# Performance work log

Hardware: AMD Instinct MI355X
Metric: run time of the kernel (lower is better)

## Reference

```python
import jax, jax.numpy as jnp
import numpy as np

B, N, C, S, H = 16, 4096, 512, 8, 8


def setup_inputs() -> dict:
    key = jax.random.key(0)
    ks = jax.random.split(key, 5)
    return {
        "x": jax.random.normal(ks[0], (B, N, C), jnp.float32),
        "w_sum": jax.random.normal(ks[1], (S, C), jnp.float32) * 0.02,
        "b_sum": jnp.zeros((S,), jnp.float32),
        "w_qkv": jax.random.normal(ks[2], (3 * C, C), jnp.float32) * 0.02,
        "w_cross": jax.random.normal(ks[3], (S, S), jnp.float32) * 0.02,
        "gamma": jnp.ones((C,), jnp.float32),
        "beta": jnp.zeros((C,), jnp.float32),
    }


def reference(x, w_sum, b_sum, w_qkv, w_cross, gamma, beta):
    Bx, Nx, Cx = x.shape
    hd = Cx // H
    scale = hd ** -0.5

    space_attn = x @ w_sum.T + b_sum                       # (B,N,S)
    # torch .view(B,C,N) on a (B,N,C) contiguous tensor is a memory
    # reinterpretation, NOT a transpose -> reshape then transpose.
    x_e = x.reshape(Bx, Cx, Nx).transpose(0, 2, 1)         # (B,N,C) reinterpreted
    sa = space_attn.reshape(Bx, S, Nx).transpose(0, 2, 1)  # (B,N,S) reinterpreted

    sa_soft = jax.nn.softmax(sa, axis=1)                   # softmax over N
    # broadcast multiply -> (B,N,S,C), top-1 over N == max over N
    tokens = jnp.max(sa_soft[:, :, :, None] * x_e[:, :, None, :], axis=1)  # (B,S,C)

    qkv = (tokens @ w_qkv.T).reshape(Bx, S, 3, H, hd).transpose(2, 0, 3, 1, 4)
    q, k, v = qkv[0], qkv[1], qkv[2]                       # (B,H,S,hd)
    attn = jax.nn.softmax(jnp.einsum('bhqd,bhkd->bhqk', q, k) * scale, axis=-1)
    asp = jnp.einsum('bhqk,bhkd->bhqd', attn, v)           # (B,H,S,hd)
    asp = asp.transpose(0, 2, 1, 3).reshape(Bx, S, Cx)     # (B,S,C)
    asp = (asp.transpose(0, 2, 1) @ w_cross.T).transpose(0, 2, 1)  # (B,S,C)

    # final mixing uses the PRE-softmax reinterpreted space_attn (as in torch)
    out = jnp.einsum('bns,bsc->bnc', sa, asp)              # (B,N,C)

    mu = out.mean(-1, keepdims=True)
    var = out.var(-1, keepdims=True)
    out = (out - mu) / jnp.sqrt(var + 1e-5) * gamma + beta
    return out + x
```

## Files before the change

### kernel.cpp

```cpp
#include <hip/hip_runtime.h>

#define Bc 16
#define Nc 4096
#define Cc 512
#define Sc 8
#define PERB (Nc*Sc)
#define WP 516

__device__ __forceinline__ float wave_max(float v){
  #pragma unroll
  for (int o = 32; o; o >>= 1) v = fmaxf(v, __shfl_xor(v, o, 64));
  return v;
}
__device__ __forceinline__ float wave_sum(float v){
  #pragma unroll
  for (int o = 32; o; o >>= 1) v += __shfl_xor(v, o, 64);
  return v;
}

__global__ __launch_bounds__(256) void k1_space_attn(
    const float* __restrict__ x, const float* __restrict__ w_sum,
    const float* __restrict__ b_sum, float* __restrict__ SA)
{
  __shared__ float wlds[Sc*WP];
  __shared__ float blds[Sc];
  int t = threadIdx.x;
  for (int i = t; i < Sc*Cc; i += 256) {
    int s = i >> 9, c = i & 511;
    wlds[s*WP + c] = w_sum[i];
  }
  if (t < Sc) blds[t] = b_sum[t];
  __syncthreads();
  int wave = t >> 6, lane = t & 63;
  int s = lane & 7, rsub = lane >> 3;
  long row = (long)blockIdx.x * 32 + wave*8 + rsub;
  const float* xr = x + row * Cc;
  float acc = blds[s];
  #pragma unroll 4
  for (int c = 0; c < Cc; c += 8) {
    float4 x0 = *(const float4*)(xr + c);
    float4 x1 = *(const float4*)(xr + c + 4);
    float4 w0 = *(const float4*)&wlds[s*WP + c];
    float4 w1 = *(const float4*)&wlds[s*WP + c + 4];
    acc = fmaf(x0.x, w0.x, acc);
    acc = fmaf(x0.y, w0.y, acc);
    acc = fmaf(x0.z, w0.z, acc);
    acc = fmaf(x0.w, w0.w, acc);
    acc = fmaf(x1.x, w1.x, acc);
    acc = fmaf(x1.y, w1.y, acc);
    acc = fmaf(x1.z, w1.z, acc);
    acc = fmaf(x1.w, w1.w, acc);
  }
  SA[row*8 + s] = acc;
}

__global__ __launch_bounds__(256) void k2_softmax(
    const float* __restrict__ SA, float* __restrict__ W)
{
  int b = blockIdx.x >> 3, s = blockIdx.x & 7;
  const float* p = SA + (long)b*PERB + s*Nc;
  float* wp = W + (long)b*PERB + s*Nc;
  int t = threadIdx.x, wave = t >> 6, lane = t & 63;
  __shared__ float red[4];
  float v[16];
  float m = -3.4e38f;
  #pragma unroll
  for (int i = 0; i < 16; i++) { v[i] = p[t + 256*i]; m = fmaxf(m, v[i]); }
  m = wave_max(m);
  if (lane == 0) red[wave] = m;
  __syncthreads();
  m = fmaxf(fmaxf(red[0], red[1]), fmaxf(red[2], red[3]));
  __syncthreads();
  float sum = 0.f;
  #pragma unroll
  for (int i = 0; i < 16; i++) { v[i] = __expf(v[i] - m); sum += v[i]; }
  sum = wave_sum(sum);
  if (lane == 0) red[wave] = sum;
  __syncthreads();
  sum = red[0] + red[1] + red[2] + red[3];
  float inv = 1.f / sum;
  #pragma unroll
  for (int i = 0; i < 16; i++) wp[t + 256*i] = v[i] * inv;
}

__global__ __launch_bounds__(256) void k3_tokens(
    const float* __restrict__ x, const float* __restrict__ W, float* __restrict__ TOK)
{
  int b = blockIdx.x >> 6;
  int c0 = (blockIdx.x & 63) * 8;
  int t = threadIdx.x, wave = t >> 6, lane = t & 63;
  const float* Wb = W + (long)b*PERB;
  const float* xb = x + (long)b*Nc*Cc;
  float acc[8][8];
  #pragma unroll
  for (int cc = 0; cc < 8; cc++)
    #pragma unroll
    for (int s = 0; s < 8; s++) acc[cc][s] = -3.4e38f;
  int nbase = wave * 1024 + 4*lane;
  #pragma unroll
  for (int step = 0; step < 4; step++) {
    int n = nbase + step*256;
    float4 wv[8];
    #pragma unroll
    for (int s = 0; s < 8; s++) wv[s] = *(const float4*)(Wb + s*Nc + n);
    #pragma unroll
    for (int cc = 0; cc < 8; cc++) {
      float4 xv = *(const float4*)(xb + (c0+cc)*Nc + n);
      #pragma unroll
      for (int s = 0; s < 8; s++) {
        float p0 = wv[s].x * xv.x, p1 = wv[s].y * xv.y;
        float p2 = wv[s].z * xv.z, p3 = wv[s].w * xv.w;
        acc[cc][s] = fmaxf(acc[cc][s], fmaxf(fmaxf(p0, p1), fmaxf(p2, p3)));
      }
    }
  }
  #pragma unroll
  for (int o = 32; o; o >>= 1) {
    #pragma unroll
    for (int cc = 0; cc < 8; cc++)
      #pragma unroll
      for (int s = 0; s < 8; s++)
        acc[cc][s] = fmaxf(acc[cc][s], __shfl_xor(acc[cc][s], o, 64));
  }
  __shared__ float part[4][64];
  if (lane == 0) {
    #pragma unroll
    for (int cc = 0; cc < 8; cc++)
      #pragma unroll
      for (int s = 0; s < 8; s++) part[wave][cc*8+s] = acc[cc][s];
  }
  __syncthreads();
  if (t < 64) {
    float m = fmaxf(fmaxf(part[0][t], part[1][t]), fmaxf(part[2][t], part[3][t]));
    int cc = t >> 3, s = t & 7;
    TOK[b*4096 + s*Cc + c0 + cc] = m;
  }
}

__global__ __launch_bounds__(256) void k4a_qkv(
    const float* __restrict__ TOK, const float* __restrict__ w_qkv, float* __restrict__ QKV)
{
  int b = blockIdx.x / 48;
  int j0 = (blockIdx.x % 48) * 32;
  __shared__ float tl[Sc*WP];
  int t = threadIdx.x;
  for (int i = t; i < Sc*Cc; i += 256) {
    int s = i >> 9, c = i & 511;
    tl[s*WP + c] = TOK[b*4096 + i];
  }
  __syncthreads();
  int wave = t >> 6, lane = t & 63;
  int s = lane & 7, jj = lane >> 3;
  int j = j0 + wave*8 + jj;
  const float* wr = w_qkv + (long)j * Cc;
  float acc = 0.f;
  #pragma unroll 4
  for (int c = 0; c < Cc; c += 8) {
    float4 w0 = *(const float4*)(wr + c);
    float4 w1 = *(const float4*)(wr + c + 4);
    float4 t0 = *(const float4*)&tl[s*WP + c];
    float4 t1 = *(const float4*)&tl[s*WP + c + 4];
    acc = fmaf(w0.x, t0.x, acc);
    acc = fmaf(w0.y, t0.y, acc);
    acc = fmaf(w0.z, t0.z, acc);
    acc = fmaf(w0.w, t0.w, acc);
    acc = fmaf(w1.x, t1.x, acc);
    acc = fmaf(w1.y, t1.y, acc);
    acc = fmaf(w1.z, t1.z, acc);
    acc = fmaf(w1.w, t1.w, acc);
  }
  QKV[b*12288 + s*1536 + j] = acc;
}

__global__ __launch_bounds__(256) void k4b_attn(
    const float* __restrict__ QKV, const float* __restrict__ w_cross, float* __restrict__ ASP2)
{
  int b = blockIdx.x, t = threadIdx.x;
  __shared__ float qkv[12288];
  __shared__ float attn[512];
  __shared__ float asp[4096];
  __shared__ float wc[64];
  for (int i = t*4; i < 12288; i += 1024)
    *(float4*)&qkv[i] = *(const float4*)&QKV[b*12288 + i];
  if (t < 64) wc[t] = w_cross[t];
  __syncthreads();
  for (int idx = t; idx < 512; idx += 256) {
    int h = idx >> 6, i = (idx >> 3) & 7, j = idx & 7;
    float sc = 0.f;
    #pragma unroll 8
    for (int d = 0; d < 64; d++)
      sc = fmaf(qkv[i*1536 + h*64 + d], qkv[j*1536 + 512 + h*64 + d], sc);
    attn[idx] = sc * 0.125f;
  }
  __syncthreads();
  if (t < 64) {
    int base = t * 8;
    float m = -3.4e38f;
    #pragma unroll
    for (int j = 0; j < 8; j++) m = fmaxf(m, attn[base+j]);
    float sum = 0.f;
    #pragma unroll
    for (int j = 0; j < 8; j++) { float e = __expf(attn[base+j] - m); attn[base+j] = e; sum += e; }
    float inv = 1.f / sum;
    #pragma unroll
    for (int j = 0; j < 8; j++) attn[base+j] *= inv;
  }
  __syncthreads();
  for (int idx = t; idx < 4096; idx += 256) {
    int i = idx >> 9, c = idx & 511, h = c >> 6;
    float a = 0.f;
    #pragma unroll
    for (int j = 0; j < 8; j++)
      a = fmaf(attn[h*64 + i*8 + j], qkv[j*1536 + 1024 + c], a);
    asp[idx] = a;
  }
  __syncthreads();
  for (int idx = t; idx < 4096; idx += 256) {
    int s = idx >> 9, c = idx & 511;
    float a = 0.f;
    #pragma unroll
    for (int j = 0; j < 8; j++)
      a = fmaf(wc[s*8 + j], asp[j*512 + c], a);
    ASP2[b*4096 + idx] = a;
  }
}

__global__ __launch_bounds__(256) void k5_out(
    const float* __restrict__ SA, const float* __restrict__ ASP2,
    const float* __restrict__ x, const float* __restrict__ gamma,
    const float* __restrict__ beta, float* __restrict__ out)
{
  int b = blockIdx.x >> 7;
  int n0 = (blockIdx.x & 127) * 32;
  int t = threadIdx.x, wave = t >> 6, lane = t & 63;
  int c0 = lane * 8;
  float a2[8][8];
  #pragma unroll
  for (int s = 0; s < 8; s++) {
    float4 p0 = *(const float4*)(ASP2 + b*4096 + s*Cc + c0);
    float4 p1 = *(const float4*)(ASP2 + b*4096 + s*Cc + c0 + 4);
    a2[s][0]=p0.x; a2[s][1]=p0.y; a2[s][2]=p0.z; a2[s][3]=p0.w;
    a2[s][4]=p1.x; a2[s][5]=p1.y; a2[s][6]=p1.z; a2[s][7]=p1.w;
  }
  float g[8], be[8];
  {
    float4 g0 = *(const float4*)(gamma + c0);
    float4 g1 = *(const float4*)(gamma + c0 + 4);
    float4 b0 = *(const float4*)(beta + c0);
    float4 b1 = *(const float4*)(beta + c0 + 4);
    g[0]=g0.x; g[1]=g0.y; g[2]=g0.z; g[3]=g0.w;
    g[4]=g1.x; g[5]=g1.y; g[6]=g1.z; g[7]=g1.w;
    be[0]=b0.x; be[1]=b0.y; be[2]=b0.z; be[3]=b0.w;
    be[4]=b1.x; be[5]=b1.y; be[6]=b1.z; be[7]=b1.w;
  }
  __shared__ float salds[32*8];
  if (t < 256) {
    int s = t >> 5, nl = t & 31;
    salds[nl*8 + s] = SA[(long)b*PERB + s*Nc + n0 + nl];
  }
  __syncthreads();
  const float inv512 = 1.f/512.f;
  #pragma unroll 2
  for (int nl = wave*8; nl < wave*8 + 8; nl++) {
    int n = n0 + nl;
    float sa8[8];
    #pragma unroll
    for (int s = 0; s < 8; s++) sa8[s] = salds[nl*8 + s];
    long row = (long)b*Nc + n;
    float4 x0 = *(const float4*)(x + row*Cc + c0);
    float4 x1 = *(const float4*)(x + row*Cc + c0 + 4);
    float o[8];
    #pragma unroll
    for (int i = 0; i < 8; i++) {
      float v = 0.f;
      #pragma unroll
      for (int s = 0; s < 8; s++) v = fmaf(sa8[s], a2[s][i], v);
      o[i] = v;
    }
    float sum = 0.f, sq = 0.f;
    #pragma unroll
    for (int i = 0; i < 8; i++) { sum += o[i]; sq = fmaf(o[i], o[i], sq); }
    #pragma unroll
    for (int off = 32; off; off >>= 1) {
      sum += __shfl_xor(sum, off, 64);
      sq  += __shfl_xor(sq,  off, 64);
    }
    float mu = sum * inv512;
    float var = sq * inv512 - mu*mu;
    float r = rsqrtf(var + 1e-5f);
    float xf[8];
    xf[0]=x0.x; xf[1]=x0.y; xf[2]=x0.z; xf[3]=x0.w;
    xf[4]=x1.x; xf[5]=x1.y; xf[6]=x1.z; xf[7]=x1.w;
    float4 o0, o1;
    o0.x = (o[0] - mu) * r * g[0] + be[0] + xf[0];
    o0.y = (o[1] - mu) * r * g[1] + be[1] + xf[1];
    o0.z = (o[2] - mu) * r * g[2] + be[2] + xf[2];
    o0.w = (o[3] - mu) * r * g[3] + be[3] + xf[3];
    o1.x = (o[4] - mu) * r * g[4] + be[4] + xf[4];
    o1.y = (o[5] - mu) * r * g[5] + be[5] + xf[5];
    o1.z = (o[6] - mu) * r * g[6] + be[6] + xf[6];
    o1.w = (o[7] - mu) * r * g[7] + be[7] + xf[7];
    *(float4*)(out + row*Cc + c0) = o0;
    *(float4*)(out + row*Cc + c0 + 4) = o1;
  }
}

extern "C" void kernel_launch(void* const* d_in, const int* in_sizes, int n_in,
                              void* d_out, int out_size, void* d_ws, size_t ws_size,
                              hipStream_t stream) {
  const float* x       = (const float*)d_in[0];
  const float* w_sum   = (const float*)d_in[1];
  const float* b_sum   = (const float*)d_in[2];
  const float* w_qkv   = (const float*)d_in[3];
  const float* w_cross = (const float*)d_in[4];
  const float* gamma   = (const float*)d_in[5];
  const float* beta    = (const float*)d_in[6];
  float* out = (float*)d_out;
  float* ws = (float*)d_ws;
  float* SA   = ws;
  float* W    = ws + 524288;
  float* TOK  = ws + 1048576;
  float* QKV  = ws + 1114112;
  float* ASP2 = ws + 1310720;

  k1_space_attn<<<2048, 256, 0, stream>>>(x, w_sum, b_sum, SA);
  k2_softmax<<<128, 256, 0, stream>>>(SA, W);
  k3_tokens<<<1024, 256, 0, stream>>>(x, W, TOK);
  k4a_qkv<<<768, 256, 0, stream>>>(TOK, w_qkv, QKV);
  k4b_attn<<<16, 256, 0, stream>>>(QKV, w_cross, ASP2);
  k5_out<<<2048, 256, 0, stream>>>(SA, ASP2, x, gamma, beta, out);
}
```

Baseline: 346.7 us.

## Fold softmax normalization into token max and fuse QKV with per-head attention

The softmax kernel now writes only the per-(batch, slot) max and inverse sum. The token kernel recomputes the exponentials from the raw scores and applies the 1/sum scaling after the max, which is valid because the scale is positive. This removes writing and re-reading the normalized weight array. Separately, the QKV projection and attention kernels are merged into one kernel per (batch, head) that computes only that head's q, k and v slices, dropping the QKV round trip and one launch. The costs are extra exp work inside the token kernel and only 128 blocks of 512 threads for the fused projection.

```diff
diff --git a/kernel.cpp b/kernel.cpp
--- a/kernel.cpp
+++ b/kernel.cpp
@@ -54,12 +54,11 @@
   SA[row*8 + s] = acc;
 }
 
-__global__ __launch_bounds__(256) void k2_softmax(
-    const float* __restrict__ SA, float* __restrict__ W)
+__global__ __launch_bounds__(256) void k2_stats(
+    const float* __restrict__ SA, float* __restrict__ ML)
 {
   int b = blockIdx.x >> 3, s = blockIdx.x & 7;
   const float* p = SA + (long)b*PERB + s*Nc;
-  float* wp = W + (long)b*PERB + s*Nc;
   int t = threadIdx.x, wave = t >> 6, lane = t & 63;
   __shared__ float red[4];
   float v[16];
@@ -73,24 +72,29 @@
   __syncthreads();
   float sum = 0.f;
   #pragma unroll
-  for (int i = 0; i < 16; i++) { v[i] = __expf(v[i] - m); sum += v[i]; }
+  for (int i = 0; i < 16; i++) sum += __expf(v[i] - m);
   sum = wave_sum(sum);
   if (lane == 0) red[wave] = sum;
   __syncthreads();
-  sum = red[0] + red[1] + red[2] + red[3];
-  float inv = 1.f / sum;
-  #pragma unroll
-  for (int i = 0; i < 16; i++) wp[t + 256*i] = v[i] * inv;
+  if (t == 0) {
+    float l = red[0] + red[1] + red[2] + red[3];
+    ML[blockIdx.x*2]     = m;
+    ML[blockIdx.x*2 + 1] = 1.f / l;
+  }
 }
 
 __global__ __launch_bounds__(256) void k3_tokens(
-    const float* __restrict__ x, const float* __restrict__ W, float* __restrict__ TOK)
+    const float* __restrict__ x, const float* __restrict__ SA,
+    const float* __restrict__ ML, float* __restrict__ TOK)
 {
   int b = blockIdx.x >> 6;
   int c0 = (blockIdx.x & 63) * 8;
   int t = threadIdx.x, wave = t >> 6, lane = t & 63;
-  const float* Wb = W + (long)b*PERB;
+  const float* SAb = SA + (long)b*PERB;
   const float* xb = x + (long)b*Nc*Cc;
+  float ms[8];
+  #pragma unroll
+  for (int s = 0; s < 8; s++) ms[s] = ML[(b*8 + s)*2];
   float acc[8][8];
   #pragma unroll
   for (int cc = 0; cc < 8; cc++)
@@ -100,16 +104,22 @@
   #pragma unroll
   for (int step = 0; step < 4; step++) {
     int n = nbase + step*256;
-    float4 wv[8];
-    #pragma unroll
-    for (int s = 0; s < 8; s++) wv[s] = *(const float4*)(Wb + s*Nc + n);
+    float4 ev[8];
+    #pragma unroll
+    for (int s = 0; s < 8; s++) {
+      float4 sa4 = *(const float4*)(SAb + s*Nc + n);
+      ev[s].x = __expf(sa4.x - ms[s]);
+      ev[s].y = __expf(sa4.y - ms[s]);
+      ev[s].z = __expf(sa4.z - ms[s]);
+      ev[s].w = __expf(sa4.w - ms[s]);
+    }
     #pragma unroll
     for (int cc = 0; cc < 8; cc++) {
       float4 xv = *(const float4*)(xb + (c0+cc)*Nc + n);
       #pragma unroll
       for (int s = 0; s < 8; s++) {
-        float p0 = wv[s].x * xv.x, p1 = wv[s].y * xv.y;
-        float p2 = wv[s].z * xv.z, p3 = wv[s].w * xv.w;
+        float p0 = ev[s].x * xv.x, p1 = ev[s].y * xv.y;
+        float p2 = ev[s].z * xv.z, p3 = ev[s].w * xv.w;
         acc[cc][s] = fmaxf(acc[cc][s], fmaxf(fmaxf(p0, p1), fmaxf(p2, p3)));
       }
     }
@@ -133,68 +143,62 @@
   if (t < 64) {
     float m = fmaxf(fmaxf(part[0][t], part[1][t]), fmaxf(part[2][t], part[3][t]));
     int cc = t >> 3, s = t & 7;
-    TOK[b*4096 + s*Cc + c0 + cc] = m;
-  }
-}
-
-__global__ __launch_bounds__(256) void k4a_qkv(
-    const float* __restrict__ TOK, const float* __restrict__ w_qkv, float* __restrict__ QKV)
-{
-  int b = blockIdx.x / 48;
-  int j0 = (blockIdx.x % 48) * 32;
+    TOK[b*4096 + s*Cc + c0 + cc] = m * ML[(b*8 + s)*2 + 1];
+  }
+}
+
+__global__ __launch_bounds__(512) void k4_attn(
+    const float* __restrict__ TOK, const float* __restrict__ w_qkv,
+    const float* __restrict__ w_cross, float* __restrict__ ASP2)
+{
+  int b = blockIdx.x >> 3, h = blockIdx.x & 7;
+  int t = threadIdx.x;
   __shared__ float tl[Sc*WP];
-  int t = threadIdx.x;
-  for (int i = t; i < Sc*Cc; i += 256) {
+  __shared__ float qk[3][8][68];
+  __shared__ float attn[64];
+  __shared__ float asp[8][68];
+  __shared__ float wc[64];
+  for (int i = t; i < Sc*Cc; i += 512) {
     int s = i >> 9, c = i & 511;
     tl[s*WP + c] = TOK[b*4096 + i];
   }
-  __syncthreads();
-  int wave = t >> 6, lane = t & 63;
-  int s = lane & 7, jj = lane >> 3;
-  int j = j0 + wave*8 + jj;
-  const float* wr = w_qkv + (long)j * Cc;
-  float acc = 0.f;
-  #pragma unroll 4
-  for (int c = 0; c < Cc; c += 8) {
-    float4 w0 = *(const float4*)(wr + c);
-    float4 w1 = *(const float4*)(wr + c + 4);
-    float4 t0 = *(const float4*)&tl[s*WP + c];
-    float4 t1 = *(const float4*)&tl[s*WP + c + 4];
-    acc = fmaf(w0.x, t0.x, acc);
-    acc = fmaf(w0.y, t0.y, acc);
-    acc = fmaf(w0.z, t0.z, acc);
-    acc = fmaf(w0.w, t0.w, acc);
-    acc = fmaf(w1.x, t1.x, acc);
-    acc = fmaf(w1.y, t1.y, acc);
-    acc = fmaf(w1.z, t1.z, acc);
-    acc = fmaf(w1.w, t1.w, acc);
-  }
-  QKV[b*12288 + s*1536 + j] = acc;
-}
-
-__global__ __launch_bounds__(256) void k4b_attn(
-    const float* __restrict__ QKV, const float* __restrict__ w_cross, float* __restrict__ ASP2)
-{
-  int b = blockIdx.x, t = threadIdx.x;
-  __shared__ float qkv[12288];
-  __shared__ float attn[512];
-  __shared__ float asp[4096];
-  __shared__ float wc[64];
-  for (int i = t*4; i < 12288; i += 1024)
-    *(float4*)&qkv[i] = *(const float4*)&QKV[b*12288 + i];
   if (t < 64) wc[t] = w_cross[t];
   __syncthreads();
-  for (int idx = t; idx < 512; idx += 256) {
-    int h = idx >> 6, i = (idx >> 3) & 7, j = idx & 7;
+  #pragma unroll
+  for (int r = 0; r < 3; r++) {
+    int idx = t + 512*r;
+    int row = idx >> 3, s = idx & 7;
+    int sect = row >> 6, d = row & 63;
+    const float* wr = w_qkv + (long)(sect*512 + h*64 + d) * Cc;
+    float acc = 0.f;
+    #pragma unroll 4
+    for (int c = 0; c < Cc; c += 8) {
+      float4 w0 = *(const float4*)(wr + c);
+      float4 w1 = *(const float4*)(wr + c + 4);
+      float4 t0 = *(const float4*)&tl[s*WP + c];
+      float4 t1 = *(const float4*)&tl[s*WP + c + 4];
+      acc = fmaf(w0.x, t0.x, acc);
+      acc = fmaf(w0.y, t0.y, acc);
+      acc = fmaf(w0.z, t0.z, acc);
+      acc = fmaf(w0.w, t0.w, acc);
+      acc = fmaf(w1.x, t1.x, acc);
+      acc = fmaf(w1.y, t1.y, acc);
+      acc = fmaf(w1.z, t1.z, acc);
+      acc = fmaf(w1.w, t1.w, acc);
+    }
+    qk[sect][s][d] = acc;
+  }
+  __syncthreads();
+  if (t < 64) {
+    int i = t >> 3, j = t & 7;
     float sc = 0.f;
-    #pragma unroll 8
-    for (int d = 0; d < 64; d++)
-      sc = fmaf(qkv[i*1536 + h*64 + d], qkv[j*1536 + 512 + h*64 + d], sc);
-    attn[idx] = sc * 0.125f;
-  }
-  __syncthreads();
-  if (t < 64) {
-    int base = t * 8;
+    #pragma unroll
+    for (int d = 0; d < 64; d++) sc = fmaf(qk[0][i][d], qk[1][j][d], sc);
+    attn[t] = sc * 0.125f;
+  }
+  __syncthreads();
+  if (t < 8) {
+    int base = t*8;
     float m = -3.4e38f;
     #pragma unroll
     for (int j = 0; j < 8; j++) m = fmaxf(m, attn[base+j]);
@@ -206,22 +210,20 @@
     for (int j = 0; j < 8; j++) attn[base+j] *= inv;
   }
   __syncthreads();
-  for (int idx = t; idx < 4096; idx += 256) {
-    int i = idx >> 9, c = idx & 511, h = c >> 6;
+  {
+    int i = t >> 6, d = t & 63;
     float a = 0.f;
     #pragma unroll
-    for (int j = 0; j < 8; j++)
-      a = fmaf(attn[h*64 + i*8 + j], qkv[j*1536 + 1024 + c], a);
-    asp[idx] = a;
-  }
-  __syncthreads();
-  for (int idx = t; idx < 4096; idx += 256) {
-    int s = idx >> 9, c = idx & 511;
+    for (int j = 0; j < 8; j++) a = fmaf(attn[i*8+j], qk[2][j][d], a);
+    asp[i][d] = a;
+  }
+  __syncthreads();
+  {
+    int s = t >> 6, d = t & 63;
     float a = 0.f;
     #pragma unroll
-    for (int j = 0; j < 8; j++)
-      a = fmaf(wc[s*8 + j], asp[j*512 + c], a);
-    ASP2[b*4096 + idx] = a;
+    for (int j = 0; j < 8; j++) a = fmaf(wc[s*8+j], asp[j][d], a);
+    ASP2[b*4096 + s*512 + h*64 + d] = a;
   }
 }
 
@@ -318,15 +320,13 @@
   float* out = (float*)d_out;
   float* ws = (float*)d_ws;
   float* SA   = ws;
-  float* W    = ws + 524288;
-  float* TOK  = ws + 1048576;
-  float* QKV  = ws + 1114112;
-  float* ASP2 = ws + 1310720;
+  float* TOK  = ws + 524288;
+  float* ASP2 = ws + 589824;
+  float* ML   = ws + 655360;
 
   k1_space_attn<<<2048, 256, 0, stream>>>(x, w_sum, b_sum, SA);
-  k2_softmax<<<128, 256, 0, stream>>>(SA, W);
-  k3_tokens<<<1024, 256, 0, stream>>>(x, W, TOK);
-  k4a_qkv<<<768, 256, 0, stream>>>(TOK, w_qkv, QKV);
-  k4b_attn<<<16, 256, 0, stream>>>(QKV, w_cross, ASP2);
+  k2_stats<<<128, 256, 0, stream>>>(SA, ML);
+  k3_tokens<<<1024, 256, 0, stream>>>(x, SA, ML, TOK);
+  k4_attn<<<128, 512, 0, stream>>>(TOK, w_qkv, w_cross, ASP2);
   k5_out<<<2048, 256, 0, stream>>>(SA, ASP2, x, gamma, beta, out);
 }
```

Measured after the change: 355.9 us. 2.7% more time.
